# Performance work log

Hardware: AMD Instinct MI355X
Metric: run time of the kernel (lower is better)

The kernel has to match this reference:

```python
import jax, jax.numpy as jnp
import numpy as np

NUM_EXPERTS = 8
TOP_K = 2
ROUTE_SCALE = 1.0
DIM = 1024
HID = 1024
B, S = 2, 4096


def setup_inputs() -> dict:
    key = jax.random.key(0)
    ks = jax.random.split(key, 9)
    sc = 0.05
    return {
        "x": jax.random.normal(ks[0], (B, S, DIM), dtype=jnp.float32),
        "gate_w": jax.random.normal(ks[1], (NUM_EXPERTS, DIM), dtype=jnp.float32) * sc,
        "w1": jax.random.normal(ks[2], (NUM_EXPERTS, HID, DIM), dtype=jnp.float32) * sc,
        "w2": jax.random.normal(ks[3], (NUM_EXPERTS, DIM, HID), dtype=jnp.float32) * sc,
        "w3": jax.random.normal(ks[4], (NUM_EXPERTS, HID, DIM), dtype=jnp.float32) * sc,
        "sw1": jax.random.normal(ks[5], (HID, DIM), dtype=jnp.float32) * sc,
        "sw2": jax.random.normal(ks[6], (DIM, HID), dtype=jnp.float32) * sc,
        "sw3": jax.random.normal(ks[7], (HID, DIM), dtype=jnp.float32) * sc,
        "expert_bias": jnp.zeros((NUM_EXPERTS,), dtype=jnp.float32),
    }


def reference(x, gate_w, w1, w2, w3, sw1, sw2, sw3, expert_bias):
    bs, slen, dim = x.shape
    xf = x.reshape(-1, dim)                      # [T, D]

    # ---- router (sigmoid scoring, top-k over scores + bias, gather true scores) ----
    scores = jax.nn.sigmoid((xf @ gate_w.T).astype(jnp.float32))   # [T, E]
    _, sel = jax.lax.top_k(scores + expert_bias[None, :], TOP_K)    # [T, K] int32
    top_scores = jnp.take_along_axis(scores, sel, axis=1) * ROUTE_SCALE  # [T, K]

    # ---- stable sort token-slots by chosen expert (dispatch permutation) ----
    flat_sel = sel.reshape(-1)                       # [T*K]
    order = jnp.argsort(flat_sel, stable=True)       # [T*K]
    scores_sorted = top_scores.reshape(-1)[order]    # [T*K]
    tok_idx = order // TOP_K                         # source token per slot
    expert_ids = flat_sel[order]                     # sorted expert id per slot

    routed = xf[tok_idx]                             # gather [T*K, D]
    # score_before_experts=True: scale inputs by routing score
    routed = (routed.astype(jnp.float32) * scores_sorted[:, None]).astype(x.dtype)

    # ---- grouped expert GLU MLP (loop over fixed expert count, masked) ----
    out_r = jnp.zeros_like(routed)
    for e in range(NUM_EXPERTS):
        m = (expert_ids == e)[:, None]
        h = jax.nn.silu(routed @ w1[e].T) * (routed @ w3[e].T)   # [T*K, H]
        out_r = out_r + jnp.where(m, h @ w2[e].T, jnp.zeros((), routed.dtype))

    # ---- shared expert on all tokens ----
    shared = (jax.nn.silu(xf @ sw1.T) * (xf @ sw3.T)) @ sw2.T    # [T, D]

    # NOTE: original code multiplies by routing scores again after experts
    # (in addition to score_before_experts) -- replicated faithfully.
    out_r = (out_r.astype(jnp.float32) * scores_sorted[:, None]).astype(x.dtype)

    out = shared.at[tok_idx].add(out_r)              # scatter-add combine
    return out.reshape(bs, slen, dim)
```

## Files before the change

### kernel.cpp

```cpp
#include <hip/hip_runtime.h>
#include <stdint.h>

typedef unsigned short u16;
typedef unsigned int u32;

#define T_TOK 8192
#define DIMSZ 1024
#define HIDSZ 1024
#define NE 8
#define NSLOT (T_TOK * 2)
#define NPAD (NSLOT + 1024)

typedef __attribute__((ext_vector_type(8))) __bf16 bf16x8;
typedef __attribute__((ext_vector_type(16))) float f32x16;

#define MFMA32(a, b, c) __builtin_amdgcn_mfma_f32_32x32x16_bf16(a, b, c, 0, 0, 0)

__device__ __forceinline__ size_t ablk(int pos, int c) {
  return ((((size_t)(pos >> 7) * 32 + (c >> 5)) * 4 + ((c >> 3) & 3)) * 128 +
          (pos & 127)) * 8 + (c & 7);
}

__device__ __forceinline__ u16 f2bf(float f) {
  u32 u = __builtin_bit_cast(u32, f);
  u += 0x7FFFu + ((u >> 16) & 1u);
  return (u16)(u >> 16);
}
__device__ __forceinline__ float bflo(u32 v) { return __builtin_bit_cast(float, v << 16); }
__device__ __forceinline__ float bfhi(u32 v) { return __builtin_bit_cast(float, v & 0xffff0000u); }
__device__ __forceinline__ u32 pack2(float a, float b) {
  return (u32)f2bf(a) | ((u32)f2bf(b) << 16);
}
__device__ __forceinline__ float silu_f(float v) { return v / (1.f + expf(-v)); }

__device__ __forceinline__ void gload16(const void* g, void* l) {
  __builtin_amdgcn_global_load_lds(
      (const __attribute__((address_space(1))) unsigned int*)g,
      (__attribute__((address_space(3))) unsigned int*)l, 16, 0, 0);
}

#define PIPE_SYNC(N) asm volatile("s_waitcnt vmcnt(" #N ")\n\ts_barrier" ::: "memory")

__global__ __launch_bounds__(256) void convert_blocked(
    const float* __restrict__ s0, const float* __restrict__ s1,
    const float* __restrict__ s2, const float* __restrict__ ss0,
    const float* __restrict__ ss1, const float* __restrict__ ss2,
    u16* __restrict__ d0, u16* __restrict__ d1, u16* __restrict__ d2,
    u16* __restrict__ ds0, u16* __restrict__ ds1, u16* __restrict__ ds2) {
  __shared__ u16 lt[2048];
  int t = blockIdx.x;
  const float* s;
  u16* d;
  if (t < NE * 16 * 32) {
    s = (blockIdx.y == 0) ? s0 : (blockIdx.y == 1) ? s1 : s2;
    d = (blockIdx.y == 0) ? d0 : (blockIdx.y == 1) ? d1 : d2;
  } else {
    t -= NE * 16 * 32;
    s = (blockIdx.y == 0) ? ss0 : (blockIdx.y == 1) ? ss1 : ss2;
    d = (blockIdx.y == 0) ? ds0 : (blockIdx.y == 1) ? ds1 : ds2;
  }
  int rt = t >> 5, kt = t & 31;
  const float* sp = s + (size_t)rt * 64 * 1024 + kt * 32;
  int nl = threadIdx.x >> 2, k0 = (threadIdx.x & 3) * 8;
  float4 a = *(const float4*)(sp + (size_t)nl * 1024 + k0);
  float4 b = *(const float4*)(sp + (size_t)nl * 1024 + k0 + 4);
  uint4 p;
  p.x = pack2(a.x, a.y); p.y = pack2(a.z, a.w);
  p.z = pack2(b.x, b.y); p.w = pack2(b.z, b.w);
  *(uint4*)&lt[(threadIdx.x & 3) * 512 + nl * 8] = p;
  __syncthreads();
  *(uint4*)(d + (size_t)t * 2048 + threadIdx.x * 8) = *(const uint4*)&lt[threadIdx.x * 8];
}

__global__ __launch_bounds__(256) void router_kernel(
    const float* __restrict__ x, const float* __restrict__ gw,
    const float* __restrict__ bias, int* __restrict__ sel,
    float* __restrict__ selscore, u16* __restrict__ xb) {
  int t = blockIdx.x * 4 + (threadIdx.x >> 6);
  int lane = threadIdx.x & 63;
  float a[NE];
#pragma unroll
  for (int e = 0; e < NE; e++) a[e] = 0.f;
#pragma unroll
  for (int j = 0; j < 4; j++) {
    int c = j * 256 + lane * 4;
    float4 xv = *(const float4*)&x[(size_t)t * DIMSZ + c];
    uint2 p;
    p.x = pack2(xv.x, xv.y);
    p.y = pack2(xv.z, xv.w);
    *(uint2*)&xb[ablk(t, c)] = p;
#pragma unroll
    for (int e = 0; e < NE; e++) {
      float4 gv = *(const float4*)&gw[e * DIMSZ + c];
      a[e] = fmaf(xv.x, gv.x, fmaf(xv.y, gv.y, fmaf(xv.z, gv.z, fmaf(xv.w, gv.w, a[e]))));
    }
  }
#pragma unroll
  for (int off = 1; off < 64; off <<= 1)
#pragma unroll
    for (int e = 0; e < NE; e++) a[e] += __shfl_xor(a[e], off);
  if (lane == 0) {
    float s[NE], b[NE];
#pragma unroll
    for (int e = 0; e < NE; e++) {
      s[e] = 1.f / (1.f + expf(-a[e]));
      b[e] = s[e] + bias[e];
    }
    int e1 = 0; float v1 = b[0];
#pragma unroll
    for (int e = 1; e < NE; e++) if (b[e] > v1) { v1 = b[e]; e1 = e; }
    int e2 = -1; float v2 = -1e30f;
#pragma unroll
    for (int e = 0; e < NE; e++) if (e != e1 && b[e] > v2) { v2 = b[e]; e2 = e; }
    sel[t * 2] = e1; sel[t * 2 + 1] = e2;
    selscore[t * 2] = s[e1];
    selscore[t * 2 + 1] = s[e2];
  }
}

__global__ __launch_bounds__(1024) void rank_kernel(
    const int* __restrict__ sel, const float* __restrict__ selscore,
    int* __restrict__ slot2pos, float* __restrict__ slot_score,
    int* __restrict__ counts, int* __restrict__ offsets) {
  __shared__ int hist[NE * 1024];
  __shared__ int tot[NE];
  __shared__ int offs[NE];
  int tid = threadIdx.x;
  int sl[16];
  int h[NE];
#pragma unroll
  for (int e = 0; e < NE; e++) h[e] = 0;
#pragma unroll
  for (int j = 0; j < 4; j++) {
    int4 v = ((const int4*)sel)[tid * 4 + j];
    sl[j * 4 + 0] = v.x; sl[j * 4 + 1] = v.y;
    sl[j * 4 + 2] = v.z; sl[j * 4 + 3] = v.w;
  }
#pragma unroll
  for (int i = 0; i < 16; i++)
#pragma unroll
    for (int e = 0; e < NE; e++) h[e] += (sl[i] == e) ? 1 : 0;
#pragma unroll
  for (int e = 0; e < NE; e++) hist[e * 1024 + tid] = h[e];
  __syncthreads();
  int wid = tid >> 6, lane = tid & 63;
  if (wid < NE) {
    int e = wid;
    int vals[16];
    int lsum = 0;
#pragma unroll
    for (int i = 0; i < 16; i++) {
      int v = hist[e * 1024 + lane * 16 + i];
      vals[i] = lsum;
      lsum += v;
    }
    int incl = lsum;
#pragma unroll
    for (int off = 1; off < 64; off <<= 1) {
      int v = __shfl_up(incl, off);
      if (lane >= off) incl += v;
    }
    int excl = incl - lsum;
#pragma unroll
    for (int i = 0; i < 16; i++) hist[e * 1024 + lane * 16 + i] = vals[i] + excl;
    if (lane == 63) tot[e] = incl;
  }
  __syncthreads();
  if (tid == 0) {
    int acc = 0;
    for (int e = 0; e < NE; e++) {
      offs[e] = acc;
      offsets[e] = acc;
      counts[e] = tot[e];
      acc += (tot[e] + 127) & ~127;
    }
  }
  __syncthreads();
  int base[NE];
#pragma unroll
  for (int e = 0; e < NE; e++) base[e] = offs[e] + hist[e * 1024 + tid];
#pragma unroll
  for (int i = 0; i < 16; i++) {
    int slot = tid * 16 + i;
    int e = sl[i];
    int pos = 0;
#pragma unroll
    for (int k = 0; k < NE; k++) pos += (e == k) ? base[k] : 0;
#pragma unroll
    for (int k = 0; k < NE; k++) base[k] += (e == k) ? 1 : 0;
    slot2pos[slot] = pos;
    slot_score[pos] = selscore[slot];
  }
}

__global__ __launch_bounds__(256) void gather_kernel(
    const u16* __restrict__ xb, const float* __restrict__ selscore,
    const int* __restrict__ slot2pos, u16* __restrict__ routed) {
  int s = blockIdx.x * 4 + (threadIdx.x >> 6);
  int lane = threadIdx.x & 63;
  int pos = slot2pos[s];
  float sc = selscore[s];
  int t = s >> 1;
#pragma unroll
  for (int j = 0; j < 4; j++) {
    int c = j * 256 + lane * 4;
    uint2 v = *(const uint2*)&xb[ablk(t, c)];
    uint2 p;
    p.x = pack2(bflo(v.x) * sc, bfhi(v.x) * sc);
    p.y = pack2(bflo(v.y) * sc, bfhi(v.y) * sc);
    *(uint2*)&routed[ablk(pos, c)] = p;
  }
}

#define BUFE 12288

#define PIPE_STAGE(B)                                  \
  do {                                                 \
    u16* Lb = &lds[(B) * BUFE];                        \
    gload16(pAa, Lb + tid * 8);                        \
    gload16(pAb, Lb + 4096 + tid * 8);                 \
    gload16(pBm, Lb + 8192 + (tid >> 8) * 2048 + (tid & 255) * 8); \
    pAa += 4096; pAb += 4096; pBm += 2048;             \
  } while (0)

#define PIPE_COMPUTE(B)                                                  \
  do {                                                                   \
    _Pragma("unroll")                                                    \
    for (int c = 0; c < 2; c++) {                                        \
      int kc = 2 * c + l5;                                               \
      const u16* La = &lds[(B) * BUFE] + (wy >> 1) * 4096 + kc * 1024 +  \
                      (wy & 1) * 512;                                    \
      const u16* Lw = &lds[(B) * BUFE] + 8192 + wn * 2048 + kc * 512;    \
      bf16x8 b0 = *(const bf16x8*)&Lw[l31 * 8];                          \
      bf16x8 b1 = *(const bf16x8*)&Lw[256 + l31 * 8];                    \
      bf16x8 a0 = *(const bf16x8*)&La[l31 * 8];                          \
      acc[0][0] = MFMA32(a0, b0, acc[0][0]);                             \
      acc[0][1] = MFMA32(a0, b1, acc[0][1]);                             \
      bf16x8 a1 = *(const bf16x8*)&La[256 + l31 * 8];                    \
      acc[1][0] = MFMA32(a1, b0, acc[1][0]);                             \
      acc[1][1] = MFMA32(a1, b1, acc[1][1]);                             \
    }                                                                    \
  } while (0)

#define PIPE_PHASE(SB, CB)                  \
  PIPE_SYNC(3);                             \
  PIPE_STAGE(SB);                           \
  __builtin_amdgcn_s_setprio(1);            \
  PIPE_COMPUTE(CB);                         \
  __builtin_amdgcn_s_setprio(0);

#define PIPE_LOOP()                         \
  PIPE_STAGE(0);                            \
  PIPE_STAGE(1);                            \
  _Pragma("unroll 1")                       \
  for (int t = 0; t < 30; t += 3) {         \
    PIPE_PHASE(2, 0);                       \
    PIPE_PHASE(0, 1);                       \
    PIPE_PHASE(1, 2);                       \
  }                                         \
  PIPE_SYNC(3);                             \
  __builtin_amdgcn_s_setprio(1);            \
  PIPE_COMPUTE(0);                          \
  __builtin_amdgcn_s_setprio(0);            \
  PIPE_SYNC(0);                             \
  __builtin_amdgcn_s_setprio(1);            \
  PIPE_COMPUTE(1);                          \
  __builtin_amdgcn_s_setprio(0);

__global__ __launch_bounds__(512, 1) void dual_glu_gemm(
    const u16* __restrict__ A, const u16* __restrict__ W1,
    const u16* __restrict__ W3, u16* __restrict__ Hout,
    const u16* __restrict__ As, const u16* __restrict__ SW1,
    const u16* __restrict__ SW3, u16* __restrict__ Hs,
    const int* __restrict__ seg_off, const int* __restrict__ seg_cnt) {
  int flat = blockIdx.x + 16 * blockIdx.y + 512 * blockIdx.z;
  int xcd = flat & 7;
  int r = flat >> 3;
  int bx = r & 15;
  int s = r >> 4;
  int z, by;
  if (s < 4) { z = NE; by = xcd * 4 + s; }
  else       { z = xcd; by = s - 4; }

  const u16 *Ap, *w1p, *w3p;
  u16* Hp;
  int soff, scnt;
  if (z < NE) {
    soff = seg_off[z]; scnt = seg_cnt[z];
    Ap = A;
    w1p = W1 + (size_t)z * HIDSZ * DIMSZ;
    w3p = W3 + (size_t)z * HIDSZ * DIMSZ;
    Hp = Hout;
  } else {
    soff = 0; scnt = T_TOK;
    Ap = As; w1p = SW1; w3p = SW3;
    Hp = Hs;
  }
  int mbase = by * 256;
  if (mbase >= scnt) return;
  int hx = bx;

  __shared__ u16 lds[3 * BUFE];

  int tid = threadIdx.x;
  int lane = tid & 63;
  int wid = tid >> 6;
  int wy = wid >> 1, wn = wid & 1;
  int l5 = lane >> 5, l31 = lane & 31;

  const u16* pAa = Ap + (size_t)((soff + mbase) >> 7) * 32 * 4096 + tid * 8;
  const u16* pAb = pAa + 32 * 4096;
  const u16* pBm = ((tid >> 8) == 0 ? w1p : w3p) +
                   (size_t)hx * 32 * 2048 + (tid & 255) * 8;

  f32x16 acc[2][2];
  acc[0][0] = (f32x16)0.f; acc[0][1] = (f32x16)0.f;
  acc[1][0] = (f32x16)0.f; acc[1][1] = (f32x16)0.f;

  PIPE_LOOP();

  __syncthreads();
  float* ex = (float*)lds;
  if (wn == 0) {
#pragma unroll
    for (int i = 0; i < 2; i++)
#pragma unroll
      for (int j = 0; j < 2; j++)
#pragma unroll
        for (int r2 = 0; r2 < 16; r2++) {
          int rowl = wy * 64 + i * 32 + (r2 & 3) + 8 * (r2 >> 2) + 4 * l5;
          ex[rowl * 64 + j * 32 + l31] = acc[i][j][r2];
        }
  }
  __syncthreads();
  if (wn == 1) {
#pragma unroll
    for (int i = 0; i < 2; i++)
#pragma unroll
      for (int j = 0; j < 2; j++)
#pragma unroll
        for (int r2 = 0; r2 < 16; r2++) {
          int rowl = wy * 64 + i * 32 + (r2 & 3) + 8 * (r2 >> 2) + 4 * l5;
          int grow = mbase + rowl;
          if (grow < scnt) {
            float h1 = ex[rowl * 64 + j * 32 + l31];
            Hp[ablk(soff + grow, hx * 64 + j * 32 + l31)] =
                f2bf(silu_f(h1) * acc[i][j][r2]);
          }
        }
  }
}

__global__ __launch_bounds__(512, 1) void gemm2_kernel(
    const u16* __restrict__ A, const u16* __restrict__ W, u16* __restrict__ OutB,
    const u16* __restrict__ As, const u16* __restrict__ SW, float* __restrict__ OutF,
    const float* __restrict__ scale, const int* __restrict__ seg_off,
    const int* __restrict__ seg_cnt) {
  int flat = blockIdx.x + 8 * blockIdx.y + 256 * blockIdx.z;
  int xcd = flat & 7;
  int r = flat >> 3;
  int bx = r & 7;
  int s = r >> 3;
  int z, by;
  if (s < 4) { z = NE; by = xcd * 4 + s; }
  else       { z = xcd; by = s - 4; }

  const u16 *Ap, *wp;
  int soff, scnt;
  if (z < NE) {
    soff = seg_off[z]; scnt = seg_cnt[z];
    Ap = A; wp = W + (size_t)z * DIMSZ * HIDSZ;
  } else {
    soff = 0; scnt = T_TOK;
    Ap = As; wp = SW;
  }
  int mbase = by * 256;
  if (mbase >= scnt) return;
  int nbase = bx * 128;

  __shared__ u16 lds[3 * BUFE];

  int tid = threadIdx.x;
  int lane = tid & 63;
  int wid = tid >> 6;
  int wy = wid >> 1, wn = wid & 1;
  int l5 = lane >> 5, l31 = lane & 31;

  const u16* pAa = Ap + (size_t)((soff + mbase) >> 7) * 32 * 4096 + tid * 8;
  const u16* pAb = pAa + 32 * 4096;
  const u16* pBm = wp + (size_t)((nbase >> 6) + (tid >> 8)) * 32 * 2048 +
                   (tid & 255) * 8;

  f32x16 acc[2][2];
  acc[0][0] = (f32x16)0.f; acc[0][1] = (f32x16)0.f;
  acc[1][0] = (f32x16)0.f; acc[1][1] = (f32x16)0.f;

  PIPE_LOOP();

#pragma unroll
  for (int i = 0; i < 2; i++)
#pragma unroll
    for (int j = 0; j < 2; j++) {
      int colg = nbase + wn * 64 + j * 32 + l31;
#pragma unroll
      for (int r2 = 0; r2 < 16; r2++) {
        int rowl = (r2 & 3) + 8 * (r2 >> 2) + 4 * l5;
        int grow = mbase + wy * 64 + i * 32 + rowl;
        if (grow < scnt) {
          size_t idx = (size_t)(soff + grow) * DIMSZ + colg;
          if (z < NE) {
            OutB[idx] = f2bf(acc[i][j][r2] * scale[soff + grow]);
          } else {
            OutF[idx] = acc[i][j][r2];
          }
        }
      }
    }
}

__global__ __launch_bounds__(256) void combine_kernel(
    float* __restrict__ out, const u16* __restrict__ Orb,
    const int* __restrict__ slot2pos) {
  int t = blockIdx.x;
  int d = threadIdx.x * 4;
  int p0 = slot2pos[t * 2];
  int p1 = slot2pos[t * 2 + 1];
  float4 o = *(float4*)&out[(size_t)t * DIMSZ + d];
  uint2 a = *(const uint2*)&Orb[(size_t)p0 * DIMSZ + d];
  uint2 b = *(const uint2*)&Orb[(size_t)p1 * DIMSZ + d];
  o.x += bflo(a.x) + bflo(b.x);
  o.y += bfhi(a.x) + bfhi(b.x);
  o.z += bflo(a.y) + bflo(b.y);
  o.w += bfhi(a.y) + bfhi(b.y);
  *(float4*)&out[(size_t)t * DIMSZ + d] = o;
}

extern "C" void kernel_launch(void* const* d_in, const int* in_sizes, int n_in,
                              void* d_out, int out_size, void* d_ws, size_t ws_size,
                              hipStream_t stream) {
  const float* x = (const float*)d_in[0];
  const float* gw = (const float*)d_in[1];
  const float* w1 = (const float*)d_in[2];
  const float* w2 = (const float*)d_in[3];
  const float* w3 = (const float*)d_in[4];
  const float* sw1 = (const float*)d_in[5];
  const float* sw2 = (const float*)d_in[6];
  const float* sw3 = (const float*)d_in[7];
  const float* bias = (const float*)d_in[8];
  float* out = (float*)d_out;

  uint8_t* ws = (uint8_t*)d_ws;
  size_t off = 0;
  auto alloc = [&](size_t b) { size_t o = off; off += (b + 255) & ~(size_t)255; return o; };

  size_t ctrl = alloc(256);
  int* counts = (int*)(ws + ctrl);
  int* offsets = counts + 16;
  int* sel = (int*)(ws + alloc((size_t)NSLOT * 4));
  float* selscore = (float*)(ws + alloc((size_t)NSLOT * 4));
  float* slot_score = (float*)(ws + alloc((size_t)NPAD * 4));
  int* slot2pos = (int*)(ws + alloc((size_t)NSLOT * 4));
  u16* xb = (u16*)(ws + alloc((size_t)T_TOK * DIMSZ * 2));
  u16* routed = (u16*)(ws + alloc((size_t)NPAD * DIMSZ * 2));
  u16* Hbuf = (u16*)(ws + alloc((size_t)NPAD * HIDSZ * 2));
  u16* Orb = (u16*)(ws + alloc((size_t)NPAD * DIMSZ * 2));
  u16* Hs = (u16*)(ws + alloc((size_t)T_TOK * HIDSZ * 2));
  u16* w1b = (u16*)(ws + alloc((size_t)NE * HIDSZ * DIMSZ * 2));
  u16* w2b = (u16*)(ws + alloc((size_t)NE * DIMSZ * HIDSZ * 2));
  u16* w3b = (u16*)(ws + alloc((size_t)NE * HIDSZ * DIMSZ * 2));
  u16* sw1b = (u16*)(ws + alloc((size_t)HIDSZ * DIMSZ * 2));
  u16* sw2b = (u16*)(ws + alloc((size_t)DIMSZ * HIDSZ * 2));
  u16* sw3b = (u16*)(ws + alloc((size_t)HIDSZ * DIMSZ * 2));

  convert_blocked<<<dim3((NE + 1) * 16 * 32, 3), 256, 0, stream>>>(
      w1, w2, w3, sw1, sw2, sw3, w1b, w2b, w3b, sw1b, sw2b, sw3b);

  router_kernel<<<T_TOK / 4, 256, 0, stream>>>(x, gw, bias, sel, selscore, xb);
  rank_kernel<<<1, 1024, 0, stream>>>(sel, selscore, slot2pos, slot_score,
                                      counts, offsets);
  gather_kernel<<<NSLOT / 4, 256, 0, stream>>>(xb, selscore, slot2pos, routed);

  dual_glu_gemm<<<dim3(16, 32, NE + 1), 512, 0, stream>>>(
      routed, w1b, w3b, Hbuf, xb, sw1b, sw3b, Hs, offsets, counts);
  gemm2_kernel<<<dim3(8, 32, NE + 1), 512, 0, stream>>>(
      Hbuf, w2b, Orb, Hs, sw2b, out, slot_score, offsets, counts);

  combine_kernel<<<T_TOK, 256, 0, stream>>>(out, Orb, slot2pos);
}
```

Measured before the change: 486.5 us.

## Double GEMM block tiles to 256x256 with 1024-thread workgroups

Both grouped GEMM kernels now use 1024-thread blocks (16 waves in a 4x4 arrangement) and cover twice as many output columns per block. The per-stage load plan changes to one A load and one B load per thread, and the LDS buffer grows accordingly. The GLU epilogue exchange is split into two row-halves. The goal is more reuse of each A/B tile per LDS byte and fewer redundant loads of activations. The cost is half as many blocks, which risks lower occupancy and worse tail balance across CUs, plus heavier register and LDS use.

```diff
diff --git a/kernel.cpp b/kernel.cpp
--- a/kernel.cpp
+++ b/kernel.cpp
@@ -212,15 +212,14 @@
   }
 }
 
-#define BUFE 12288
+#define BUFE 16384
 
 #define PIPE_STAGE(B)                                  \
   do {                                                 \
     u16* Lb = &lds[(B) * BUFE];                        \
-    gload16(pAa, Lb + tid * 8);                        \
-    gload16(pAb, Lb + 4096 + tid * 8);                 \
-    gload16(pBm, Lb + 8192 + (tid >> 8) * 2048 + (tid & 255) * 8); \
-    pAa += 4096; pAb += 4096; pBm += 2048;             \
+    gload16(pA_, Lb + tid * 8);                        \
+    gload16(pBm, Lb + 8192 + tid * 8);                 \
+    pA_ += 4096; pBm += 2048;                          \
   } while (0)
 
 #define PIPE_COMPUTE(B)                                                  \
@@ -243,7 +242,7 @@
   } while (0)
 
 #define PIPE_PHASE(SB, CB)                  \
-  PIPE_SYNC(3);                             \
+  PIPE_SYNC(2);                             \
   PIPE_STAGE(SB);                           \
   __builtin_amdgcn_s_setprio(1);            \
   PIPE_COMPUTE(CB);                         \
@@ -258,7 +257,7 @@
     PIPE_PHASE(0, 1);                       \
     PIPE_PHASE(1, 2);                       \
   }                                         \
-  PIPE_SYNC(3);                             \
+  PIPE_SYNC(2);                             \
   __builtin_amdgcn_s_setprio(1);            \
   PIPE_COMPUTE(0);                          \
   __builtin_amdgcn_s_setprio(0);            \
@@ -267,17 +266,17 @@
   PIPE_COMPUTE(1);                          \
   __builtin_amdgcn_s_setprio(0);
 
-__global__ __launch_bounds__(512, 1) void dual_glu_gemm(
+__global__ __launch_bounds__(1024, 1) void dual_glu_gemm(
     const u16* __restrict__ A, const u16* __restrict__ W1,
     const u16* __restrict__ W3, u16* __restrict__ Hout,
     const u16* __restrict__ As, const u16* __restrict__ SW1,
     const u16* __restrict__ SW3, u16* __restrict__ Hs,
     const int* __restrict__ seg_off, const int* __restrict__ seg_cnt) {
-  int flat = blockIdx.x + 16 * blockIdx.y + 512 * blockIdx.z;
+  int flat = blockIdx.x + 8 * blockIdx.y + 256 * blockIdx.z;
   int xcd = flat & 7;
   int r = flat >> 3;
-  int bx = r & 15;
-  int s = r >> 4;
+  int bx = r & 7;
+  int s = r >> 3;
   int z, by;
   if (s < 4) { z = NE; by = xcd * 4 + s; }
   else       { z = xcd; by = s - 4; }
@@ -305,13 +304,15 @@
   int tid = threadIdx.x;
   int lane = tid & 63;
   int wid = tid >> 6;
-  int wy = wid >> 1, wn = wid & 1;
+  int wy = wid >> 2, wn = wid & 3;
   int l5 = lane >> 5, l31 = lane & 31;
 
-  const u16* pAa = Ap + (size_t)((soff + mbase) >> 7) * 32 * 4096 + tid * 8;
-  const u16* pAb = pAa + 32 * 4096;
-  const u16* pBm = ((tid >> 8) == 0 ? w1p : w3p) +
-                   (size_t)hx * 32 * 2048 + (tid & 255) * 8;
+  const u16* pA_ = Ap +
+      (size_t)(((soff + mbase) >> 7) + (tid >> 9)) * 32 * 4096 +
+      (tid & 511) * 8;
+  int bu = tid >> 8;
+  const u16* pBm = ((bu < 2) ? w1p : w3p) +
+                   (size_t)(hx * 2 + (bu & 1)) * 32 * 2048 + (tid & 255) * 8;
 
   f32x16 acc[2][2];
   acc[0][0] = (f32x16)0.f; acc[0][1] = (f32x16)0.f;
@@ -319,48 +320,50 @@
 
   PIPE_LOOP();
 
-  __syncthreads();
   float* ex = (float*)lds;
-  if (wn == 0) {
-#pragma unroll
-    for (int i = 0; i < 2; i++)
-#pragma unroll
-      for (int j = 0; j < 2; j++)
-#pragma unroll
-        for (int r2 = 0; r2 < 16; r2++) {
-          int rowl = wy * 64 + i * 32 + (r2 & 3) + 8 * (r2 >> 2) + 4 * l5;
-          ex[rowl * 64 + j * 32 + l31] = acc[i][j][r2];
-        }
-  }
-  __syncthreads();
-  if (wn == 1) {
-#pragma unroll
-    for (int i = 0; i < 2; i++)
-#pragma unroll
-      for (int j = 0; j < 2; j++)
-#pragma unroll
-        for (int r2 = 0; r2 < 16; r2++) {
-          int rowl = wy * 64 + i * 32 + (r2 & 3) + 8 * (r2 >> 2) + 4 * l5;
-          int grow = mbase + rowl;
-          if (grow < scnt) {
-            float h1 = ex[rowl * 64 + j * 32 + l31];
-            Hp[ablk(soff + grow, hx * 64 + j * 32 + l31)] =
-                f2bf(silu_f(h1) * acc[i][j][r2]);
+  for (int rr = 0; rr < 2; rr++) {
+    __syncthreads();
+    if ((wy >> 1) == rr && wn < 2) {
+#pragma unroll
+      for (int i = 0; i < 2; i++)
+#pragma unroll
+        for (int j = 0; j < 2; j++)
+#pragma unroll
+          for (int r2 = 0; r2 < 16; r2++) {
+            int rl = (wy & 1) * 64 + i * 32 + (r2 & 3) + 8 * (r2 >> 2) + 4 * l5;
+            ex[rl * 128 + wn * 64 + j * 32 + l31] = acc[i][j][r2];
           }
-        }
-  }
-}
-
-__global__ __launch_bounds__(512, 1) void gemm2_kernel(
+    }
+    __syncthreads();
+    if ((wy >> 1) == rr && wn >= 2) {
+#pragma unroll
+      for (int i = 0; i < 2; i++)
+#pragma unroll
+        for (int j = 0; j < 2; j++)
+#pragma unroll
+          for (int r2 = 0; r2 < 16; r2++) {
+            int rl = (wy & 1) * 64 + i * 32 + (r2 & 3) + 8 * (r2 >> 2) + 4 * l5;
+            int grow = mbase + rr * 128 + rl;
+            if (grow < scnt) {
+              float h1 = ex[rl * 128 + (wn - 2) * 64 + j * 32 + l31];
+              Hp[ablk(soff + grow, hx * 128 + (wn - 2) * 64 + j * 32 + l31)] =
+                  f2bf(silu_f(h1) * acc[i][j][r2]);
+            }
+          }
+    }
+  }
+}
+
+__global__ __launch_bounds__(1024, 1) void gemm2_kernel(
     const u16* __restrict__ A, const u16* __restrict__ W, u16* __restrict__ OutB,
     const u16* __restrict__ As, const u16* __restrict__ SW, float* __restrict__ OutF,
     const float* __restrict__ scale, const int* __restrict__ seg_off,
     const int* __restrict__ seg_cnt) {
-  int flat = blockIdx.x + 8 * blockIdx.y + 256 * blockIdx.z;
+  int flat = blockIdx.x + 4 * blockIdx.y + 128 * blockIdx.z;
   int xcd = flat & 7;
   int r = flat >> 3;
-  int bx = r & 7;
-  int s = r >> 3;
+  int bx = r & 3;
+  int s = r >> 2;
   int z, by;
   if (s < 4) { z = NE; by = xcd * 4 + s; }
   else       { z = xcd; by = s - 4; }
@@ -376,19 +379,21 @@
   }
   int mbase = by * 256;
   if (mbase >= scnt) return;
-  int nbase = bx * 128;
+  int nbase = bx * 256;
 
   __shared__ u16 lds[3 * BUFE];
 
   int tid = threadIdx.x;
   int lane = tid & 63;
   int wid = tid >> 6;
-  int wy = wid >> 1, wn = wid & 1;
+  int wy = wid >> 2, wn = wid & 3;
   int l5 = lane >> 5, l31 = lane & 31;
 
-  const u16* pAa = Ap + (size_t)((soff + mbase) >> 7) * 32 * 4096 + tid * 8;
-  const u16* pAb = pAa + 32 * 4096;
-  const u16* pBm = wp + (size_t)((nbase >> 6) + (tid >> 8)) * 32 * 2048 +
+  const u16* pA_ = Ap +
+      (size_t)(((soff + mbase) >> 7) + (tid >> 9)) * 32 * 4096 +
+      (tid & 511) * 8;
+  int bu = tid >> 8;
+  const u16* pBm = wp + (size_t)((nbase >> 6) + bu) * 32 * 2048 +
                    (tid & 255) * 8;
 
   f32x16 acc[2][2];
@@ -480,9 +485,9 @@
                                       counts, offsets);
   gather_kernel<<<NSLOT / 4, 256, 0, stream>>>(xb, selscore, slot2pos, routed);
 
-  dual_glu_gemm<<<dim3(16, 32, NE + 1), 512, 0, stream>>>(
+  dual_glu_gemm<<<dim3(8, 32, NE + 1), 1024, 0, stream>>>(
       routed, w1b, w3b, Hbuf, xb, sw1b, sw3b, Hs, offsets, counts);
-  gemm2_kernel<<<dim3(8, 32, NE + 1), 512, 0, stream>>>(
+  gemm2_kernel<<<dim3(4, 32, NE + 1), 1024, 0, stream>>>(
       Hbuf, w2b, Orb, Hs, sw2b, out, slot_score, offsets, counts);
 
   combine_kernel<<<T_TOK, 256, 0, stream>>>(out, Orb, slot2pos);
```

New measurement: 755.9 us. 1.55x slower.
